# Optimization experiments

Hardware: AMD Instinct MI355X
Metric: run time of the kernel (lower is better)

Reference implementation:

```python
import jax, jax.numpy as jnp
import numpy as np

B, P, N, D = 64, 16384, 64, 2


def setup_inputs() -> dict:
    key = jax.random.key(0)
    k1, k2, k3 = jax.random.split(key, 3)
    batch = jax.random.uniform(k1, (B, P, D), dtype=jnp.float32)
    not_dummy_points = jnp.ones((B, P), dtype=jnp.float32)
    # learned parameters (match torch init: centers ~ U[0,1), sharpness = 3)
    centers = jax.random.uniform(k2, (N, D), dtype=jnp.float32)
    sharpness = jnp.ones((N, D), dtype=jnp.float32) * 3.0
    return {"batch": batch, "not_dummy_points": not_dummy_points,
            "centers": centers, "sharpness": sharpness}


def reference(batch, not_dummy_points, centers, sharpness):
    # diff: [B, N, P, D] via broadcasting (torch materializes this via cat/stack)
    diff = centers[None, :, None, :] - batch[:, None, :, :]
    # Gaussian RBF exponent: sum_d sharpness[n,d] * diff^2
    expo = jnp.sum(sharpness[None, :, None, :] * diff * diff, axis=-1)  # [B,N,P]
    w = jnp.exp(-expo) * not_dummy_points[:, None, :]                   # masked RBF
    out = jnp.sum(w, axis=-1)  # [B, N] masked sum pooling over points
    return jnp.squeeze(out)
```

## Files before the change

### kernel.cpp

```cpp
#include <hip/hip_runtime.h>


#if __has_builtin(__builtin_amdgcn_exp2f)
#define EXP2(x) __builtin_amdgcn_exp2f(x)
#else
#define EXP2(x) exp2f(x)
#endif

constexpr int BATCH  = 64;
constexpr int P      = 16384;
constexpr int N      = 64;
constexpr int CHUNKS = 16;
constexpr int CHUNK  = P / CHUNKS;
constexpr int BLOCK  = 256;
constexpr int WPTS   = CHUNK / 4;

__global__ __launch_bounds__(BLOCK) void slayer_rbf(
    const float* __restrict__ batch,
    const float* __restrict__ mask,
    const float* __restrict__ centers,
    const float* __restrict__ sharp,
    float* __restrict__ out)
{
    __shared__ float sx0[CHUNK];
    __shared__ float sx1[CHUNK];
    __shared__ float smk[CHUNK];
    __shared__ float red[4][N];

    const int blk   = blockIdx.x;
    const int b     = blk >> 4;
    const int chunk = blk & (CHUNKS - 1);
    const int tid   = threadIdx.x;

    const float4* bp = (const float4*)(batch + ((size_t)b * P + (size_t)chunk * CHUNK) * 2);
    #pragma unroll
    for (int i = tid; i < CHUNK / 2; i += BLOCK) {
        float4 v = bp[i];
        sx0[2 * i]     = v.x; sx1[2 * i]     = v.y;
        sx0[2 * i + 1] = v.z; sx1[2 * i + 1] = v.w;
    }
    const float4* mp = (const float4*)(mask + (size_t)b * P + (size_t)chunk * CHUNK);
    #pragma unroll
    for (int i = tid; i < CHUNK / 4; i += BLOCK) {
        float4 v = mp[i];
        smk[4 * i]     = v.x; smk[4 * i + 1] = v.y;
        smk[4 * i + 2] = v.z; smk[4 * i + 3] = v.w;
    }

    const int lane = tid & 63;
    const float c0 = centers[2 * lane], c1 = centers[2 * lane + 1];
    const float s0 = sharp[2 * lane],  s1 = sharp[2 * lane + 1];
    const float L  = 1.4426950408889634f;
    const float C0 = -L * s0, C1 = -L * s1;
    const float B0 = -2.0f * C0 * c0, B1 = -2.0f * C1 * c1;
    const float A  = C0 * c0 * c0 + C1 * c1 * c1;

    __syncthreads();

    const int wave = tid >> 6;
    const int p0   = wave * WPTS;
    float acc0 = 0.f, acc1 = 0.f, acc2 = 0.f, acc3 = 0.f;
    for (int p = p0; p < p0 + WPTS; p += 4) {
        float xa = sx0[p + 0], ya = sx1[p + 0], ma = smk[p + 0];
        float xb = sx0[p + 1], yb = sx1[p + 1], mb = smk[p + 1];
        float xc = sx0[p + 2], yc = sx1[p + 2], mc = smk[p + 2];
        float xd = sx0[p + 3], yd = sx1[p + 3], md = smk[p + 3];
        float ta = fmaf(xa, fmaf(C0, xa, B0), fmaf(ya, fmaf(C1, ya, B1), A));
        float tb = fmaf(xb, fmaf(C0, xb, B0), fmaf(yb, fmaf(C1, yb, B1), A));
        float tc = fmaf(xc, fmaf(C0, xc, B0), fmaf(yc, fmaf(C1, yc, B1), A));
        float td = fmaf(xd, fmaf(C0, xd, B0), fmaf(yd, fmaf(C1, yd, B1), A));
        acc0 = fmaf(ma, EXP2(ta), acc0);
        acc1 = fmaf(mb, EXP2(tb), acc1);
        acc2 = fmaf(mc, EXP2(tc), acc2);
        acc3 = fmaf(md, EXP2(td), acc3);
    }
    float acc = (acc0 + acc1) + (acc2 + acc3);

    red[wave][lane] = acc;
    __syncthreads();
    if (tid < N) {
        float s = red[0][tid] + red[1][tid] + red[2][tid] + red[3][tid];
        atomicAdd(&out[b * N + tid], s);
    }
}

extern "C" void kernel_launch(void* const* d_in, const int* in_sizes, int n_in,
                              void* d_out, int out_size, void* d_ws, size_t ws_size,
                              hipStream_t stream) {
    const float* batch   = (const float*)d_in[0];
    const float* mask    = (const float*)d_in[1];
    const float* centers = (const float*)d_in[2];
    const float* sharp   = (const float*)d_in[3];
    float* out = (float*)d_out;

    hipMemsetAsync(out, 0, (size_t)out_size * sizeof(float), stream);
    slayer_rbf<<<BATCH * CHUNKS, BLOCK, 0, stream>>>(batch, mask, centers, sharp, out);
}
```

Baseline: 79.44 us.

## Read points directly from global memory and replace atomics with two-stage reduction

```diff
diff --git a/kernel.cpp b/kernel.cpp
--- a/kernel.cpp
+++ b/kernel.cpp
@@ -15,39 +15,21 @@
 constexpr int BLOCK  = 256;
 constexpr int WPTS   = CHUNK / 4;
 
-__global__ __launch_bounds__(BLOCK) void slayer_rbf(
+__global__ __launch_bounds__(BLOCK) void slayer_stage1(
     const float* __restrict__ batch,
     const float* __restrict__ mask,
     const float* __restrict__ centers,
     const float* __restrict__ sharp,
-    float* __restrict__ out)
+    float* __restrict__ partial)
 {
-    __shared__ float sx0[CHUNK];
-    __shared__ float sx1[CHUNK];
-    __shared__ float smk[CHUNK];
     __shared__ float red[4][N];
 
-    const int blk   = blockIdx.x;
-    const int b     = blk >> 4;
-    const int chunk = blk & (CHUNKS - 1);
+    const int b     = blockIdx.x >> 4;
+    const int chunk = blockIdx.x & (CHUNKS - 1);
     const int tid   = threadIdx.x;
+    const int lane  = tid & 63;
+    const int wave  = __builtin_amdgcn_readfirstlane(tid >> 6);
 
-    const float4* bp = (const float4*)(batch + ((size_t)b * P + (size_t)chunk * CHUNK) * 2);
-    #pragma unroll
-    for (int i = tid; i < CHUNK / 2; i += BLOCK) {
-        float4 v = bp[i];
-        sx0[2 * i]     = v.x; sx1[2 * i]     = v.y;
-        sx0[2 * i + 1] = v.z; sx1[2 * i + 1] = v.w;
-    }
-    const float4* mp = (const float4*)(mask + (size_t)b * P + (size_t)chunk * CHUNK);
-    #pragma unroll
-    for (int i = tid; i < CHUNK / 4; i += BLOCK) {
-        float4 v = mp[i];
-        smk[4 * i]     = v.x; smk[4 * i + 1] = v.y;
-        smk[4 * i + 2] = v.z; smk[4 * i + 3] = v.w;
-    }
-
-    const int lane = tid & 63;
     const float c0 = centers[2 * lane], c1 = centers[2 * lane + 1];
     const float s0 = sharp[2 * lane],  s1 = sharp[2 * lane + 1];
     const float L  = 1.4426950408889634f;
@@ -55,24 +37,24 @@
     const float B0 = -2.0f * C0 * c0, B1 = -2.0f * C1 * c1;
     const float A  = C0 * c0 * c0 + C1 * c1 * c1;
 
-    __syncthreads();
+    const size_t pbase = (size_t)b * P + (size_t)chunk * CHUNK + (size_t)wave * WPTS;
+    const float4* __restrict__ xy = (const float4*)(batch + pbase * 2);
+    const float4* __restrict__ mk = (const float4*)(mask + pbase);
 
-    const int wave = tid >> 6;
-    const int p0   = wave * WPTS;
     float acc0 = 0.f, acc1 = 0.f, acc2 = 0.f, acc3 = 0.f;
-    for (int p = p0; p < p0 + WPTS; p += 4) {
-        float xa = sx0[p + 0], ya = sx1[p + 0], ma = smk[p + 0];
-        float xb = sx0[p + 1], yb = sx1[p + 1], mb = smk[p + 1];
-        float xc = sx0[p + 2], yc = sx1[p + 2], mc = smk[p + 2];
-        float xd = sx0[p + 3], yd = sx1[p + 3], md = smk[p + 3];
-        float ta = fmaf(xa, fmaf(C0, xa, B0), fmaf(ya, fmaf(C1, ya, B1), A));
-        float tb = fmaf(xb, fmaf(C0, xb, B0), fmaf(yb, fmaf(C1, yb, B1), A));
-        float tc = fmaf(xc, fmaf(C0, xc, B0), fmaf(yc, fmaf(C1, yc, B1), A));
-        float td = fmaf(xd, fmaf(C0, xd, B0), fmaf(yd, fmaf(C1, yd, B1), A));
-        acc0 = fmaf(ma, EXP2(ta), acc0);
-        acc1 = fmaf(mb, EXP2(tb), acc1);
-        acc2 = fmaf(mc, EXP2(tc), acc2);
-        acc3 = fmaf(md, EXP2(td), acc3);
+    #pragma unroll 4
+    for (int g = 0; g < WPTS / 4; ++g) {
+        float4 v0 = xy[2 * g];
+        float4 v1 = xy[2 * g + 1];
+        float4 m  = mk[g];
+        float ta = fmaf(v0.x, fmaf(C0, v0.x, B0), fmaf(v0.y, fmaf(C1, v0.y, B1), A));
+        float tb = fmaf(v0.z, fmaf(C0, v0.z, B0), fmaf(v0.w, fmaf(C1, v0.w, B1), A));
+        float tc = fmaf(v1.x, fmaf(C0, v1.x, B0), fmaf(v1.y, fmaf(C1, v1.y, B1), A));
+        float td = fmaf(v1.z, fmaf(C0, v1.z, B0), fmaf(v1.w, fmaf(C1, v1.w, B1), A));
+        acc0 = fmaf(m.x, EXP2(ta), acc0);
+        acc1 = fmaf(m.y, EXP2(tb), acc1);
+        acc2 = fmaf(m.z, EXP2(tc), acc2);
+        acc3 = fmaf(m.w, EXP2(td), acc3);
     }
     float acc = (acc0 + acc1) + (acc2 + acc3);
 
@@ -80,8 +62,21 @@
     __syncthreads();
     if (tid < N) {
         float s = red[0][tid] + red[1][tid] + red[2][tid] + red[3][tid];
-        atomicAdd(&out[b * N + tid], s);
+        partial[((size_t)b * CHUNKS + chunk) * N + tid] = s;
     }
+}
+
+__global__ __launch_bounds__(256) void slayer_stage2(
+    const float* __restrict__ partial,
+    float* __restrict__ out)
+{
+    const int idx = blockIdx.x * 256 + threadIdx.x;
+    const int b = idx >> 6, n = idx & 63;
+    float s = 0.f;
+    #pragma unroll
+    for (int c = 0; c < CHUNKS; ++c)
+        s += partial[((size_t)b * CHUNKS + c) * N + n];
+    out[idx] = s;
 }
 
 extern "C" void kernel_launch(void* const* d_in, const int* in_sizes, int n_in,
@@ -91,8 +86,9 @@
     const float* mask    = (const float*)d_in[1];
     const float* centers = (const float*)d_in[2];
     const float* sharp   = (const float*)d_in[3];
-    float* out = (float*)d_out;
+    float* out     = (float*)d_out;
+    float* partial = (float*)d_ws;
 
-    hipMemsetAsync(out, 0, (size_t)out_size * sizeof(float), stream);
-    slayer_rbf<<<BATCH * CHUNKS, BLOCK, 0, stream>>>(batch, mask, centers, sharp, out);
+    slayer_stage1<<<BATCH * CHUNKS, BLOCK, 0, stream>>>(batch, mask, centers, sharp, partial);
+    slayer_stage2<<<(BATCH * N) / 256, 256, 0, stream>>>(partial, out);
 }
```

Result: no change. 80.69 us (+1.6%).
